# Kernel tuning notes

Measured on AMD Instinct MI355X. Metric: run time of the kernel, lower is better.

## Reference

```python
import jax, jax.numpy as jnp
import numpy as np

B, LQ, LK = 4, 512, 512
DQ, DC, H = 256, 256, 128


def setup_inputs() -> dict:
    key = jax.random.key(0)
    ks = jax.random.split(key, 8)
    s = lambda d: 1.0 / np.sqrt(d)
    return {
        "query": jax.random.normal(ks[0], (B, LQ, DQ), jnp.float32),
        "context": jax.random.normal(ks[1], (B, LK, DC), jnp.float32),
        "Wq": jax.random.uniform(ks[2], (H, DQ), jnp.float32, -s(DQ), s(DQ)),
        "bq": jax.random.uniform(ks[3], (H,), jnp.float32, -s(DQ), s(DQ)),
        "Wc": jax.random.uniform(ks[4], (H, DC), jnp.float32, -s(DC), s(DC)),
        "bc": jax.random.uniform(ks[5], (H,), jnp.float32, -s(DC), s(DC)),
        "Wv": jax.random.uniform(ks[6], (1, H), jnp.float32, -s(H), s(H)),
        "bv": jax.random.uniform(ks[7], (1,), jnp.float32, -s(H), s(H)),
    }


def reference(query, context, Wq, bq, Wc, bc, Wv, bv):
    # [B,Lq,H] and [B,Lk,H]
    qp = jnp.einsum("bqd,hd->bqh", query, Wq) + bq
    cp = jnp.einsum("bkd,hd->bkh", context, Wc) + bc
    # NOTE: original torch code adds context_proj twice (faithful reproduction)
    kk = qp[:, :, None, :] + 2.0 * cp[:, None, :, :]  # [B,Lq,Lk,H]
    scores = jnp.einsum("bqkh,h->bqk", jnp.tanh(kk), Wv[0]) + bv[0]
    attn = jax.nn.softmax(scores, axis=-1)  # softmax over Lk
    return jnp.einsum("bqk,bkd->bqd", attn, context)  # [B,Lq,Dc]
```

## Files before the change

### kernel.cpp

```cpp
#include <hip/hip_runtime.h>

#define B 4
#define LQ 512
#define LK 512
#define DQ 256
#define DC 256
#define H 128


__global__ __launch_bounds__(256) void ca_wt_kernel(
    const float* __restrict__ Wq, const float* __restrict__ Wc,
    float* __restrict__ WqT4, float* __restrict__ WcT4)
{
    const int blk = blockIdx.x;
    const bool is_q = blk < 128;
    const float* __restrict__ src = is_q ? Wq : Wc;
    float* __restrict__ dst = is_q ? WqT4 : WcT4;
    const int idx = ((is_q ? blk : blk - 128) << 8) + threadIdx.x;
    const int h = idx >> 8;
    const int d = idx & 255;
    dst[(((d >> 2) * H + h) << 2) + (d & 3)] = src[idx];
}

__global__ __launch_bounds__(256, 4) void ca_proj_kernel(
    const float* __restrict__ query, const float* __restrict__ context,
    const float* __restrict__ WqT4, const float* __restrict__ WcT4,
    const float* __restrict__ bq, const float* __restrict__ bc,
    float* __restrict__ Eq, float* __restrict__ EcT)
{
    const int t = threadIdx.x;
    const int blk = blockIdx.x;
    const bool is_q = blk < (B * LQ / 8);
    const int row0 = (is_q ? blk : blk - (B * LQ / 8)) * 8;
    const float* __restrict__ src = is_q ? query : context;
    const float4* __restrict__ w4 = (const float4*)(is_q ? WqT4 : WcT4);

    const int h = t & 127;
    const int rg = __builtin_amdgcn_readfirstlane(t >> 7);

    const float* __restrict__ x0p = src + (size_t)(row0 + rg    ) * DQ;
    const float* __restrict__ x1p = src + (size_t)(row0 + rg + 2) * DQ;
    const float* __restrict__ x2p = src + (size_t)(row0 + rg + 4) * DQ;
    const float* __restrict__ x3p = src + (size_t)(row0 + rg + 6) * DQ;

    float acc0 = 0.f, acc1 = 0.f, acc2 = 0.f, acc3 = 0.f;
#pragma unroll 4
    for (int d4 = 0; d4 < DQ / 4; ++d4) {
        const float4 w  = w4[d4 * H + h];
        const float4 x0 = *(const float4*)(x0p + d4 * 4);
        const float4 x1 = *(const float4*)(x1p + d4 * 4);
        const float4 x2 = *(const float4*)(x2p + d4 * 4);
        const float4 x3 = *(const float4*)(x3p + d4 * 4);
        acc0 = fmaf(w.x, x0.x, acc0); acc0 = fmaf(w.y, x0.y, acc0);
        acc0 = fmaf(w.z, x0.z, acc0); acc0 = fmaf(w.w, x0.w, acc0);
        acc1 = fmaf(w.x, x1.x, acc1); acc1 = fmaf(w.y, x1.y, acc1);
        acc1 = fmaf(w.z, x1.z, acc1); acc1 = fmaf(w.w, x1.w, acc1);
        acc2 = fmaf(w.x, x2.x, acc2); acc2 = fmaf(w.y, x2.y, acc2);
        acc2 = fmaf(w.z, x2.z, acc2); acc2 = fmaf(w.w, x2.w, acc2);
        acc3 = fmaf(w.x, x3.x, acc3); acc3 = fmaf(w.y, x3.y, acc3);
        acc3 = fmaf(w.z, x3.z, acc3); acc3 = fmaf(w.w, x3.w, acc3);
    }

    const float bias = (is_q ? bq : bc)[h];
    if (is_q) {
        Eq[(size_t)(row0 + rg    ) * H + h] = __expf(2.f * (acc0 + bias));
        Eq[(size_t)(row0 + rg + 2) * H + h] = __expf(2.f * (acc1 + bias));
        Eq[(size_t)(row0 + rg + 4) * H + h] = __expf(2.f * (acc2 + bias));
        Eq[(size_t)(row0 + rg + 6) * H + h] = __expf(2.f * (acc3 + bias));
    } else {
        const float e0 = __expf(4.f * (acc0 + bias));
        const float e1 = __expf(4.f * (acc1 + bias));
        const float e2 = __expf(4.f * (acc2 + bias));
        const float e3 = __expf(4.f * (acc3 + bias));
        int rc = row0 + rg;
        EcT[((size_t)(rc >> 9) * H + h) * LK + (rc & 511)] = e0; rc += 2;
        EcT[((size_t)(rc >> 9) * H + h) * LK + (rc & 511)] = e1; rc += 2;
        EcT[((size_t)(rc >> 9) * H + h) * LK + (rc & 511)] = e2; rc += 2;
        EcT[((size_t)(rc >> 9) * H + h) * LK + (rc & 511)] = e3;
    }
}

__global__ __launch_bounds__(512, 4) void ca_attn_kernel(
    const float* __restrict__ Eq, const float* __restrict__ EcT,
    const float* __restrict__ context, const float* __restrict__ Wv,
    float* __restrict__ out)
{
    __shared__ float sc[4][LK];
    __shared__ float part[8][4][DC];
    __shared__ float inv[4];

    const int t = threadIdx.x;
    const int bq0 = blockIdx.x * 4;
    const int b = bq0 / LQ;

    const float* __restrict__ ecb = EcT + (size_t)b * H * LK;
    const float* __restrict__ eqb = Eq + (size_t)bq0 * H;

    float a[4] = {0.f, 0.f, 0.f, 0.f};
#pragma unroll 4
    for (int h4 = 0; h4 < H / 4; ++h4) {
        const float4 wv = *(const float4*)(Wv  + h4 * 4);
        float4 q[4];
#pragma unroll
        for (int g = 0; g < 4; ++g)
            q[g] = *(const float4*)(eqb + g * H + h4 * 4);
        const float* __restrict__ ep = ecb + (size_t)h4 * 4 * LK + t;
        const float e0 = ep[0 * LK];
        const float e1 = ep[1 * LK];
        const float e2 = ep[2 * LK];
        const float e3 = ep[3 * LK];
        float r;
#pragma unroll
        for (int g = 0; g < 4; ++g) {
            r = __builtin_amdgcn_rcpf(fmaf(q[g].x, e0, 1.f)); a[g] = fmaf(wv.x, r, a[g]);
            r = __builtin_amdgcn_rcpf(fmaf(q[g].y, e1, 1.f)); a[g] = fmaf(wv.y, r, a[g]);
            r = __builtin_amdgcn_rcpf(fmaf(q[g].z, e2, 1.f)); a[g] = fmaf(wv.z, r, a[g]);
            r = __builtin_amdgcn_rcpf(fmaf(q[g].w, e3, 1.f)); a[g] = fmaf(wv.w, r, a[g]);
        }
    }
#pragma unroll
    for (int g = 0; g < 4; ++g) sc[g][t] = -2.f * a[g];
    __syncthreads();

    {
        const int w_id = t >> 6;
        const int lane = t & 63;
        if (w_id < 4) {
            float v[8];
#pragma unroll
            for (int i = 0; i < 8; ++i) v[i] = sc[w_id][lane + 64 * i];
            float m = v[0];
#pragma unroll
            for (int i = 1; i < 8; ++i) m = fmaxf(m, v[i]);
#pragma unroll
            for (int off = 32; off > 0; off >>= 1) m = fmaxf(m, __shfl_xor(m, off));
            float s = 0.f;
#pragma unroll
            for (int i = 0; i < 8; ++i) { v[i] = __expf(v[i] - m); s += v[i]; }
#pragma unroll
            for (int off = 32; off > 0; off >>= 1) s += __shfl_xor(s, off);
#pragma unroll
            for (int i = 0; i < 8; ++i) sc[w_id][lane + 64 * i] = v[i];
            if (lane == 0) inv[w_id] = 1.f / s;
        }
    }
    __syncthreads();

    {
        const int kh = t >> 6;
        const int d4 = (t & 63) * 4;
        const float* __restrict__ ctx = context + (size_t)b * LK * DC + d4;
        float4 o[4];
#pragma unroll
        for (int g = 0; g < 4; ++g) o[g] = make_float4(0.f, 0.f, 0.f, 0.f);
#pragma unroll 2
        for (int j = 0; j < 16; ++j) {
            const int k = kh * 64 + j * 4;
            float4 p[4];
#pragma unroll
            for (int g = 0; g < 4; ++g) p[g] = *(const float4*)&sc[g][k];
#pragma unroll
            for (int c = 0; c < 4; ++c) {
                const float4 cv = *(const float4*)(ctx + (size_t)(k + c) * DC);
                const float pc[4] = {p[0].x, p[1].x, p[2].x, p[3].x};
                const float pd[4] = {p[0].y, p[1].y, p[2].y, p[3].y};
                const float pe[4] = {p[0].z, p[1].z, p[2].z, p[3].z};
                const float pf[4] = {p[0].w, p[1].w, p[2].w, p[3].w};
                const float* sel = (c == 0) ? pc : (c == 1) ? pd : (c == 2) ? pe : pf;
#pragma unroll
                for (int g = 0; g < 4; ++g) {
                    o[g].x = fmaf(sel[g], cv.x, o[g].x);
                    o[g].y = fmaf(sel[g], cv.y, o[g].y);
                    o[g].z = fmaf(sel[g], cv.z, o[g].z);
                    o[g].w = fmaf(sel[g], cv.w, o[g].w);
                }
            }
        }
#pragma unroll
        for (int g = 0; g < 4; ++g)
            *(float4*)&part[kh][g][d4] = o[g];
    }
    __syncthreads();

    if (t < 256) {
#pragma unroll
        for (int g = 0; g < 4; ++g) {
            float s = 0.f;
#pragma unroll
            for (int kh = 0; kh < 8; ++kh) s += part[kh][g][t];
            out[(size_t)(bq0 + g) * DC + t] = s * inv[g];
        }
    }
}

extern "C" void kernel_launch(void* const* d_in, const int* in_sizes, int n_in,
                              void* d_out, int out_size, void* d_ws, size_t ws_size,
                              hipStream_t stream) {
    const float* query   = (const float*)d_in[0];
    const float* context = (const float*)d_in[1];
    const float* Wq = (const float*)d_in[2];
    const float* bq = (const float*)d_in[3];
    const float* Wc = (const float*)d_in[4];
    const float* bc = (const float*)d_in[5];
    const float* Wv = (const float*)d_in[6];
    const float* bv = (const float*)d_in[7];
    (void)bv;
    float* out = (float*)d_out;

    float* Eq   = (float*)d_ws;
    float* EcT  = Eq  + (size_t)B * LQ * H;
    float* WqT4 = EcT + (size_t)B * H * LK;
    float* WcT4 = WqT4 + (size_t)H * DQ;

    ca_wt_kernel<<<256, 256, 0, stream>>>(Wq, Wc, WqT4, WcT4);
    ca_proj_kernel<<<B * (LQ + LK) / 8, 256, 0, stream>>>(
        query, context, WqT4, WcT4, bq, bc, Eq, EcT);
    ca_attn_kernel<<<B * LQ / 4, 512, 0, stream>>>(Eq, EcT, context, Wv, out);
}
```

Baseline: 112.6 us.

## Pair reciprocals in tanh score sum and vectorize EcT layout as float4

Combines two reciprocal terms into one via a common denominator, halving the rcp count in the score loop. Stores the context exponentials in an h4-interleaved float4 layout so each thread issues one vector load, and stages Eq and Wv in shared memory. The projection kernel uses 512-thread blocks covering 16 rows. The product of two large exponentials may overflow to inf, risking NaN where the per-term form was bounded.

```diff
diff --git a/kernel.cpp b/kernel.cpp
--- a/kernel.cpp
+++ b/kernel.cpp
@@ -22,26 +22,26 @@
     dst[(((d >> 2) * H + h) << 2) + (d & 3)] = src[idx];
 }
 
-__global__ __launch_bounds__(256, 4) void ca_proj_kernel(
+__global__ __launch_bounds__(512, 4) void ca_proj_kernel(
     const float* __restrict__ query, const float* __restrict__ context,
     const float* __restrict__ WqT4, const float* __restrict__ WcT4,
     const float* __restrict__ bq, const float* __restrict__ bc,
-    float* __restrict__ Eq, float* __restrict__ EcT)
+    float* __restrict__ Eq, float* __restrict__ EcT4)
 {
     const int t = threadIdx.x;
     const int blk = blockIdx.x;
-    const bool is_q = blk < (B * LQ / 8);
-    const int row0 = (is_q ? blk : blk - (B * LQ / 8)) * 8;
+    const bool is_q = blk < (B * LQ / 16);
+    const int row0 = (is_q ? blk : blk - (B * LQ / 16)) * 16;
     const float* __restrict__ src = is_q ? query : context;
     const float4* __restrict__ w4 = (const float4*)(is_q ? WqT4 : WcT4);
 
     const int h = t & 127;
     const int rg = __builtin_amdgcn_readfirstlane(t >> 7);
 
-    const float* __restrict__ x0p = src + (size_t)(row0 + rg    ) * DQ;
-    const float* __restrict__ x1p = src + (size_t)(row0 + rg + 2) * DQ;
-    const float* __restrict__ x2p = src + (size_t)(row0 + rg + 4) * DQ;
-    const float* __restrict__ x3p = src + (size_t)(row0 + rg + 6) * DQ;
+    const float* __restrict__ x0p = src + (size_t)(row0 + rg     ) * DQ;
+    const float* __restrict__ x1p = src + (size_t)(row0 + rg +  4) * DQ;
+    const float* __restrict__ x2p = src + (size_t)(row0 + rg +  8) * DQ;
+    const float* __restrict__ x3p = src + (size_t)(row0 + rg + 12) * DQ;
 
     float acc0 = 0.f, acc1 = 0.f, acc2 = 0.f, acc3 = 0.f;
 #pragma unroll 4
@@ -63,59 +63,65 @@
 
     const float bias = (is_q ? bq : bc)[h];
     if (is_q) {
-        Eq[(size_t)(row0 + rg    ) * H + h] = __expf(2.f * (acc0 + bias));
-        Eq[(size_t)(row0 + rg + 2) * H + h] = __expf(2.f * (acc1 + bias));
-        Eq[(size_t)(row0 + rg + 4) * H + h] = __expf(2.f * (acc2 + bias));
-        Eq[(size_t)(row0 + rg + 6) * H + h] = __expf(2.f * (acc3 + bias));
+        Eq[(size_t)(row0 + rg     ) * H + h] = __expf(2.f * (acc0 + bias));
+        Eq[(size_t)(row0 + rg +  4) * H + h] = __expf(2.f * (acc1 + bias));
+        Eq[(size_t)(row0 + rg +  8) * H + h] = __expf(2.f * (acc2 + bias));
+        Eq[(size_t)(row0 + rg + 12) * H + h] = __expf(2.f * (acc3 + bias));
     } else {
-        const float e0 = __expf(4.f * (acc0 + bias));
-        const float e1 = __expf(4.f * (acc1 + bias));
-        const float e2 = __expf(4.f * (acc2 + bias));
-        const float e3 = __expf(4.f * (acc3 + bias));
-        int rc = row0 + rg;
-        EcT[((size_t)(rc >> 9) * H + h) * LK + (rc & 511)] = e0; rc += 2;
-        EcT[((size_t)(rc >> 9) * H + h) * LK + (rc & 511)] = e1; rc += 2;
-        EcT[((size_t)(rc >> 9) * H + h) * LK + (rc & 511)] = e2; rc += 2;
-        EcT[((size_t)(rc >> 9) * H + h) * LK + (rc & 511)] = e3;
+        const int h4 = h >> 2, hl = h & 3;
+        float e[4] = {__expf(4.f * (acc0 + bias)), __expf(4.f * (acc1 + bias)),
+                      __expf(4.f * (acc2 + bias)), __expf(4.f * (acc3 + bias))};
+#pragma unroll
+        for (int i = 0; i < 4; ++i) {
+            const int rc = row0 + rg + i * 4;
+            const int bb = rc >> 9, kk = rc & 511;
+            EcT4[(((size_t)(bb * 32 + h4) * LK + kk) << 2) + hl] = e[i];
+        }
     }
 }
 
 __global__ __launch_bounds__(512, 4) void ca_attn_kernel(
-    const float* __restrict__ Eq, const float* __restrict__ EcT,
+    const float* __restrict__ Eq, const float* __restrict__ EcT4,
     const float* __restrict__ context, const float* __restrict__ Wv,
     float* __restrict__ out)
 {
     __shared__ float sc[4][LK];
     __shared__ float part[8][4][DC];
+    __shared__ float eqs[4][H];
+    __shared__ float wv[H];
     __shared__ float inv[4];
 
     const int t = threadIdx.x;
     const int bq0 = blockIdx.x * 4;
     const int b = bq0 / LQ;
 
-    const float* __restrict__ ecb = EcT + (size_t)b * H * LK;
-    const float* __restrict__ eqb = Eq + (size_t)bq0 * H;
+    if (t < H) {
+        wv[t] = Wv[t];
+#pragma unroll
+        for (int g = 0; g < 4; ++g) eqs[g][t] = Eq[(size_t)(bq0 + g) * H + t];
+    }
+    __syncthreads();
+
+    const float4* __restrict__ ecb = (const float4*)EcT4 + (size_t)b * 32 * LK;
 
     float a[4] = {0.f, 0.f, 0.f, 0.f};
 #pragma unroll 4
     for (int h4 = 0; h4 < H / 4; ++h4) {
-        const float4 wv = *(const float4*)(Wv  + h4 * 4);
-        float4 q[4];
-#pragma unroll
-        for (int g = 0; g < 4; ++g)
-            q[g] = *(const float4*)(eqb + g * H + h4 * 4);
-        const float* __restrict__ ep = ecb + (size_t)h4 * 4 * LK + t;
-        const float e0 = ep[0 * LK];
-        const float e1 = ep[1 * LK];
-        const float e2 = ep[2 * LK];
-        const float e3 = ep[3 * LK];
-        float r;
+        const float4 e = ecb[h4 * LK + t];
+        const float4 w = *(const float4*)&wv[h4 * 4];
 #pragma unroll
         for (int g = 0; g < 4; ++g) {
-            r = __builtin_amdgcn_rcpf(fmaf(q[g].x, e0, 1.f)); a[g] = fmaf(wv.x, r, a[g]);
-            r = __builtin_amdgcn_rcpf(fmaf(q[g].y, e1, 1.f)); a[g] = fmaf(wv.y, r, a[g]);
-            r = __builtin_amdgcn_rcpf(fmaf(q[g].z, e2, 1.f)); a[g] = fmaf(wv.z, r, a[g]);
-            r = __builtin_amdgcn_rcpf(fmaf(q[g].w, e3, 1.f)); a[g] = fmaf(wv.w, r, a[g]);
+            const float4 q = *(const float4*)&eqs[g][h4 * 4];
+            const float A = fmaf(q.x, e.x, 1.f);
+            const float Bv = fmaf(q.y, e.y, 1.f);
+            const float C = fmaf(q.z, e.z, 1.f);
+            const float D = fmaf(q.w, e.w, 1.f);
+            float n1 = w.x * Bv; n1 = fmaf(w.y, A, n1);
+            float n2 = w.z * D;  n2 = fmaf(w.w, C, n2);
+            const float r1 = __builtin_amdgcn_rcpf(A * Bv);
+            const float r2 = __builtin_amdgcn_rcpf(C * D);
+            a[g] = fmaf(n1, r1, a[g]);
+            a[g] = fmaf(n2, r2, a[g]);
         }
     }
 #pragma unroll
@@ -208,12 +214,12 @@
     float* out = (float*)d_out;
 
     float* Eq   = (float*)d_ws;
-    float* EcT  = Eq  + (size_t)B * LQ * H;
-    float* WqT4 = EcT + (size_t)B * H * LK;
+    float* EcT4 = Eq  + (size_t)B * LQ * H;
+    float* WqT4 = EcT4 + (size_t)B * H * LK;
     float* WcT4 = WqT4 + (size_t)H * DQ;
 
     ca_wt_kernel<<<256, 256, 0, stream>>>(Wq, Wc, WqT4, WcT4);
-    ca_proj_kernel<<<B * (LQ + LK) / 8, 256, 0, stream>>>(
-        query, context, WqT4, WcT4, bq, bc, Eq, EcT);
-    ca_attn_kernel<<<B * LQ / 4, 512, 0, stream>>>(Eq, EcT, context, Wv, out);
-}
+    ca_proj_kernel<<<B * (LQ + LK) / 16, 512, 0, stream>>>(
+        query, context, WqT4, WcT4, bq, bc, Eq, EcT4);
+    ca_attn_kernel<<<B * LQ / 4, 512, 0, stream>>>(Eq, EcT4, context, Wv, out);
+}
```

Result: faster. 110.3 us (-2.0%).

## Pair reciprocals, interleave Ec by h4, and double attention block to 1024 threads

Applied to the files above, without the earlier changes.

Ec is now stored in an h4-interleaved float4 layout so each thread reads one float4 per h-group instead of four strided floats. Reciprocals are paired algebraically (w1/A + w2/B = (w1·B + w2·A)/(A·B)), which halves the rcp count. The attention block grows to 1024 threads: the H reduction is split across two halves, and the PV product is split over k and d. Softmax normalization is folded into the probabilities before the PV step. The paired product A·B could overflow for large exponents, and the 1024-thread blocks change occupancy and add an extra partial-sum pass.

```diff
diff --git a/kernel.cpp b/kernel.cpp
--- a/kernel.cpp
+++ b/kernel.cpp
@@ -26,7 +26,7 @@
     const float* __restrict__ query, const float* __restrict__ context,
     const float* __restrict__ WqT4, const float* __restrict__ WcT4,
     const float* __restrict__ bq, const float* __restrict__ bc,
-    float* __restrict__ Eq, float* __restrict__ EcT)
+    float* __restrict__ Eq, float* __restrict__ EcT4)
 {
     const int t = threadIdx.x;
     const int blk = blockIdx.x;
@@ -68,58 +68,64 @@
         Eq[(size_t)(row0 + rg + 4) * H + h] = __expf(2.f * (acc2 + bias));
         Eq[(size_t)(row0 + rg + 6) * H + h] = __expf(2.f * (acc3 + bias));
     } else {
+        const int h4 = h >> 2, hl = h & 3;
         const float e0 = __expf(4.f * (acc0 + bias));
         const float e1 = __expf(4.f * (acc1 + bias));
         const float e2 = __expf(4.f * (acc2 + bias));
         const float e3 = __expf(4.f * (acc3 + bias));
-        int rc = row0 + rg;
-        EcT[((size_t)(rc >> 9) * H + h) * LK + (rc & 511)] = e0; rc += 2;
-        EcT[((size_t)(rc >> 9) * H + h) * LK + (rc & 511)] = e1; rc += 2;
-        EcT[((size_t)(rc >> 9) * H + h) * LK + (rc & 511)] = e2; rc += 2;
-        EcT[((size_t)(rc >> 9) * H + h) * LK + (rc & 511)] = e3;
-    }
-}
-
-__global__ __launch_bounds__(512, 4) void ca_attn_kernel(
-    const float* __restrict__ Eq, const float* __restrict__ EcT,
+        const float ee[4] = {e0, e1, e2, e3};
+#pragma unroll
+        for (int i = 0; i < 4; ++i) {
+            const int rc = row0 + rg + i * 2;
+            const int bb = rc >> 9, kk = rc & 511;
+            EcT4[(((size_t)(bb * 32 + h4) * LK + kk) << 2) + hl] = ee[i];
+        }
+    }
+}
+
+__global__ __launch_bounds__(1024, 8) void ca_attn_kernel(
+    const float* __restrict__ Eq, const float* __restrict__ EcT4,
     const float* __restrict__ context, const float* __restrict__ Wv,
     float* __restrict__ out)
 {
-    __shared__ float sc[4][LK];
-    __shared__ float part[8][4][DC];
-    __shared__ float inv[4];
+    __shared__ float smem[10240];
 
     const int t = threadIdx.x;
     const int bq0 = blockIdx.x * 4;
     const int b = bq0 / LQ;
 
-    const float* __restrict__ ecb = EcT + (size_t)b * H * LK;
+    const float4* __restrict__ ecb = (const float4*)EcT4 + (size_t)b * 32 * LK;
     const float* __restrict__ eqb = Eq + (size_t)bq0 * H;
 
-    float a[4] = {0.f, 0.f, 0.f, 0.f};
-#pragma unroll 4
-    for (int h4 = 0; h4 < H / 4; ++h4) {
-        const float4 wv = *(const float4*)(Wv  + h4 * 4);
-        float4 q[4];
+    {
+        const int k  = t & 511;
+        const int hh = __builtin_amdgcn_readfirstlane(t >> 9);
+        float a[4] = {0.f, 0.f, 0.f, 0.f};
+        const int h4_0 = hh * 16;
+#pragma unroll 2
+        for (int i = 0; i < 16; ++i) {
+            const int h4 = h4_0 + i;
+            const float4 e = ecb[h4 * LK + k];
+            const float4 w = *(const float4*)(Wv + h4 * 4);
+#pragma unroll
+            for (int g = 0; g < 4; ++g) {
+                const float4 q = *(const float4*)(eqb + g * H + h4 * 4);
+                const float A  = fmaf(q.x, e.x, 1.f);
+                const float Bv = fmaf(q.y, e.y, 1.f);
+                const float C  = fmaf(q.z, e.z, 1.f);
+                const float D  = fmaf(q.w, e.w, 1.f);
+                float n1 = w.x * Bv; n1 = fmaf(w.y, A, n1);
+                float n2 = w.z * D;  n2 = fmaf(w.w, C, n2);
+                const float r1 = __builtin_amdgcn_rcpf(A * Bv);
+                const float r2 = __builtin_amdgcn_rcpf(C * D);
+                a[g] = fmaf(n1, r1, a[g]);
+                a[g] = fmaf(n2, r2, a[g]);
+            }
+        }
 #pragma unroll
         for (int g = 0; g < 4; ++g)
-            q[g] = *(const float4*)(eqb + g * H + h4 * 4);
-        const float* __restrict__ ep = ecb + (size_t)h4 * 4 * LK + t;
-        const float e0 = ep[0 * LK];
-        const float e1 = ep[1 * LK];
-        const float e2 = ep[2 * LK];
-        const float e3 = ep[3 * LK];
-        float r;
-#pragma unroll
-        for (int g = 0; g < 4; ++g) {
-            r = __builtin_amdgcn_rcpf(fmaf(q[g].x, e0, 1.f)); a[g] = fmaf(wv.x, r, a[g]);
-            r = __builtin_amdgcn_rcpf(fmaf(q[g].y, e1, 1.f)); a[g] = fmaf(wv.y, r, a[g]);
-            r = __builtin_amdgcn_rcpf(fmaf(q[g].z, e2, 1.f)); a[g] = fmaf(wv.z, r, a[g]);
-            r = __builtin_amdgcn_rcpf(fmaf(q[g].w, e3, 1.f)); a[g] = fmaf(wv.w, r, a[g]);
-        }
-    }
-#pragma unroll
-    for (int g = 0; g < 4; ++g) sc[g][t] = -2.f * a[g];
+            smem[2048 + hh * 2048 + g * 512 + k] = a[g];
+    }
     __syncthreads();
 
     {
@@ -128,7 +134,12 @@
         if (w_id < 4) {
             float v[8];
 #pragma unroll
-            for (int i = 0; i < 8; ++i) v[i] = sc[w_id][lane + 64 * i];
+            for (int i = 0; i < 8; ++i) {
+                const int k = lane + 64 * i;
+                const float p0 = smem[2048 + w_id * 512 + k];
+                const float p1 = smem[4096 + w_id * 512 + k];
+                v[i] = -2.f * (p0 + p1);
+            }
             float m = v[0];
 #pragma unroll
             for (int i = 1; i < 8; ++i) m = fmaxf(m, v[i]);
@@ -139,57 +150,53 @@
             for (int i = 0; i < 8; ++i) { v[i] = __expf(v[i] - m); s += v[i]; }
 #pragma unroll
             for (int off = 32; off > 0; off >>= 1) s += __shfl_xor(s, off);
-#pragma unroll
-            for (int i = 0; i < 8; ++i) sc[w_id][lane + 64 * i] = v[i];
-            if (lane == 0) inv[w_id] = 1.f / s;
+            const float r = 1.f / s;
+#pragma unroll
+            for (int i = 0; i < 8; ++i)
+                smem[(lane + 64 * i) * 4 + w_id] = v[i] * r;
         }
     }
     __syncthreads();
 
     {
-        const int kh = t >> 6;
-        const int d4 = (t & 63) * 4;
-        const float* __restrict__ ctx = context + (size_t)b * LK * DC + d4;
-        float4 o[4];
-#pragma unroll
-        for (int g = 0; g < 4; ++g) o[g] = make_float4(0.f, 0.f, 0.f, 0.f);
-#pragma unroll 2
-        for (int j = 0; j < 16; ++j) {
-            const int k = kh * 64 + j * 4;
-            float4 p[4];
-#pragma unroll
-            for (int g = 0; g < 4; ++g) p[g] = *(const float4*)&sc[g][k];
-#pragma unroll
-            for (int c = 0; c < 4; ++c) {
-                const float4 cv = *(const float4*)(ctx + (size_t)(k + c) * DC);
-                const float pc[4] = {p[0].x, p[1].x, p[2].x, p[3].x};
-                const float pd[4] = {p[0].y, p[1].y, p[2].y, p[3].y};
-                const float pe[4] = {p[0].z, p[1].z, p[2].z, p[3].z};
-                const float pf[4] = {p[0].w, p[1].w, p[2].w, p[3].w};
-                const float* sel = (c == 0) ? pc : (c == 1) ? pd : (c == 2) ? pe : pf;
-#pragma unroll
-                for (int g = 0; g < 4; ++g) {
-                    o[g].x = fmaf(sel[g], cv.x, o[g].x);
-                    o[g].y = fmaf(sel[g], cv.y, o[g].y);
-                    o[g].z = fmaf(sel[g], cv.z, o[g].z);
-                    o[g].w = fmaf(sel[g], cv.w, o[g].w);
-                }
+        const int w_all = t >> 6;
+        const int lane = t & 63;
+        const int kh = __builtin_amdgcn_readfirstlane(w_all & 7);
+        const int dh = __builtin_amdgcn_readfirstlane(w_all >> 3);
+        const int d0 = dh * 128 + lane * 2;
+        const float* __restrict__ ctx = context + (size_t)b * LK * DC + d0;
+        float ox[4] = {0.f, 0.f, 0.f, 0.f};
+        float oy[4] = {0.f, 0.f, 0.f, 0.f};
+#pragma unroll 4
+        for (int j = 0; j < 64; ++j) {
+            const int k = kh * 64 + j;
+            const float4 p = *(const float4*)&smem[k * 4];
+            const float2 c = *(const float2*)(ctx + (size_t)k * DC);
+            const float pl[4] = {p.x, p.y, p.z, p.w};
+#pragma unroll
+            for (int g = 0; g < 4; ++g) {
+                ox[g] = fmaf(pl[g], c.x, ox[g]);
+                oy[g] = fmaf(pl[g], c.y, oy[g]);
             }
         }
-#pragma unroll
-        for (int g = 0; g < 4; ++g)
-            *(float4*)&part[kh][g][d4] = o[g];
+        const int base = 2048 + (((kh * 2 + dh) * 4) << 7) + lane * 2;
+#pragma unroll
+        for (int g = 0; g < 4; ++g) {
+            smem[base + (g << 7) * 1 + 0] = ox[g];
+            smem[base + (g << 7) * 1 + 1] = oy[g];
+        }
     }
     __syncthreads();
 
-    if (t < 256) {
-#pragma unroll
-        for (int g = 0; g < 4; ++g) {
-            float s = 0.f;
-#pragma unroll
-            for (int kh = 0; kh < 8; ++kh) s += part[kh][g][t];
-            out[(size_t)(bq0 + g) * DC + t] = s * inv[g];
-        }
+    {
+        const int g = t >> 8;
+        const int d = t & 255;
+        const int dh = d >> 7, dl = d & 127;
+        float s = 0.f;
+#pragma unroll
+        for (int kh = 0; kh < 8; ++kh)
+            s += smem[2048 + (((kh * 2 + dh) * 4 + g) << 7) + dl];
+        out[(size_t)(bq0 + g) * DC + d] = s;
     }
 }
 
@@ -208,12 +215,12 @@
     float* out = (float*)d_out;
 
     float* Eq   = (float*)d_ws;
-    float* EcT  = Eq  + (size_t)B * LQ * H;
-    float* WqT4 = EcT + (size_t)B * H * LK;
+    float* EcT4 = Eq  + (size_t)B * LQ * H;
+    float* WqT4 = EcT4 + (size_t)B * H * LK;
     float* WcT4 = WqT4 + (size_t)H * DQ;
 
     ca_wt_kernel<<<256, 256, 0, stream>>>(Wq, Wc, WqT4, WcT4);
     ca_proj_kernel<<<B * (LQ + LK) / 8, 256, 0, stream>>>(
-        query, context, WqT4, WcT4, bq, bc, Eq, EcT);
-    ca_attn_kernel<<<B * LQ / 4, 512, 0, stream>>>(Eq, EcT, context, Wv, out);
-}
+        query, context, WqT4, WcT4, bq, bc, Eq, EcT4);
+    ca_attn_kernel<<<B * LQ / 4, 1024, 0, stream>>>(Eq, EcT4, context, Wv, out);
+}
```

Result: slower. 116.8 us (+3.8%).
